# Kernel optimization log

Hardware: AMD Instinct MI355X
Metric: run time of the kernel (lower is better)

The kernel has to match this reference:

```python
import jax, jax.numpy as jnp
import numpy as np

B, L, D, DFF, H, P, TOPK = 64, 321, 512, 2048, 8, 16, 10
LEAKY_ALPHA = 0.5

def setup_inputs() -> dict:
    ks = iter(jax.random.split(jax.random.key(0), 40))
    def w(shape):
        return jax.random.normal(next(ks), shape, dtype=jnp.float32) * 0.02
    inp = {"x": jax.random.normal(next(ks), (B, L, D), dtype=jnp.float32)}
    for name, si, so in [("attn_q", D, D), ("attn_k", D, D), ("attn_v", D, D), ("attn_o", D, D),
                         ("enc", D, D),
                         ("ff1_q", D, DFF), ("ff1_k", D, D), ("ff1_v", D, D), ("ff1_o", DFF, DFF),
                         ("ff2_q", DFF, D), ("ff2_k", DFF, DFF), ("ff2_v", DFF, DFF), ("ff2_o", D, D)]:
        inp[name + "_w"] = w((si, so))
        inp[name + "_b"] = jnp.zeros((so,), dtype=jnp.float32)
    inp["ln_g"] = jnp.ones((DFF,), dtype=jnp.float32)
    inp["ln_b"] = jnp.zeros((DFF,), dtype=jnp.float32)
    inp["n_vars"] = L
    return inp

def _gattn(x, wq, bq, wk, bk, wv, bv, wo, bo):
    Bx, Lx, Dx = x.shape
    E = Dx // H
    q = jax.nn.relu(x @ wq + bq).reshape(Bx, Lx, H, E)
    k = (x @ wk + bk).reshape(Bx, Lx, H, E)
    v = jax.nn.relu(x @ wv + bv).reshape(Bx, Lx, H, E)
    scores = jnp.einsum('blhe,bshe->bhls', q, k)  # [B,H,L,S]
    kth = jax.lax.top_k(scores, TOPK)[0][..., -1:]  # k-th largest per row
    scores = jnp.where(scores < kth, -jnp.inf, scores)
    A = jax.nn.softmax(scores * jnp.float32(1.0 / np.sqrt(E)), axis=-1)
    out = jnp.einsum('bhls,bshd->blhd', A, v).reshape(Bx, Lx, Dx)
    return out @ wo + bo, A

def _pwattn(x, wq, bq, wk, bk, wv, bv, wo, bo):
    N, S = x.shape
    pred = wq.shape[1]
    query = jax.nn.relu(x @ wq + bq)  # [N, pred]
    q = query.reshape(N, pred // P, P)
    k = (x @ wk + bk).reshape(N, S // P, P)
    v = jax.nn.relu(x @ wv + bv).reshape(N, S // P, P)
    A = jax.nn.softmax(jnp.einsum('ble,bse->bls', q, k) * jnp.float32(1.0 / np.sqrt(P)), axis=-1)
    V = jnp.einsum('bls,bse->ble', A, v).reshape(N, pred)
    return query + (V @ wo + bo)

def _layernorm(x, g, b):
    m = x.mean(-1, keepdims=True)
    v = x.var(-1, keepdims=True)
    return (x - m) * jax.lax.rsqrt(v + 1e-5) * g + b

def _forward(x, attn_q_w, attn_q_b, attn_k_w, attn_k_b, attn_v_w, attn_v_b, attn_o_w, attn_o_b,
             enc_w, enc_b,
             ff1_q_w, ff1_q_b, ff1_k_w, ff1_k_b, ff1_v_w, ff1_v_b, ff1_o_w, ff1_o_b,
             ff2_q_w, ff2_q_b, ff2_k_w, ff2_k_b, ff2_v_w, ff2_v_b, ff2_o_w, ff2_o_b,
             ln_g, ln_b, n_vars):
    new_x, A = _gattn(x, attn_q_w, attn_q_b, attn_k_w, attn_k_b, attn_v_w, attn_v_b, attn_o_w, attn_o_b)
    y = x + new_x  # Encoder residual
    y = jax.nn.leaky_relu(y, negative_slope=LEAKY_ALPHA) @ enc_w + enc_b
    y = y.reshape(-1, y.shape[-1])  # [B*L, D]
    y = _layernorm(jax.nn.elu(_pwattn(y, ff1_q_w, ff1_q_b, ff1_k_w, ff1_k_b, ff1_v_w, ff1_v_b, ff1_o_w, ff1_o_b)), ln_g, ln_b)
    y = _pwattn(y, ff2_q_w, ff2_q_b, ff2_k_w, ff2_k_b, ff2_v_w, ff2_v_b, ff2_o_w, ff2_o_b)
    y = y.reshape(-1, n_vars, y.shape[-1])
    return y, A

def reference(x, attn_q_w, attn_q_b, attn_k_w, attn_k_b, attn_v_w, attn_v_b, attn_o_w, attn_o_b,
              enc_w, enc_b,
              ff1_q_w, ff1_q_b, ff1_k_w, ff1_k_b, ff1_v_w, ff1_v_b, ff1_o_w, ff1_o_b,
              ff2_q_w, ff2_q_b, ff2_k_w, ff2_k_b, ff2_v_w, ff2_v_b, ff2_o_w, ff2_o_b,
              ln_g, ln_b, n_vars):
    return _forward(x, attn_q_w, attn_q_b, attn_k_w, attn_k_b, attn_v_w, attn_v_b, attn_o_w, attn_o_b,
                    enc_w, enc_b,
                    ff1_q_w, ff1_q_b, ff1_k_w, ff1_k_b, ff1_v_w, ff1_v_b, ff1_o_w, ff1_o_b,
                    ff2_q_w, ff2_q_b, ff2_k_w, ff2_k_b, ff2_v_w, ff2_v_b, ff2_o_w, ff2_o_b,
                    ln_g, ln_b, n_vars)
```

## Files before the change

kernel.cpp:

```cpp
#include <hip/hip_runtime.h>
#include <hip/hip_bf16.h>
#include <math.h>

#define N_ROWS 20544
#define MP     20608
#define LSEQ   321
#define BB     64
#define HH     8
#define EE     64
#define DD     512
#define DFF    2048

typedef __attribute__((ext_vector_type(8))) short bf16x8;
typedef __attribute__((ext_vector_type(4))) float f32x4;

__device__ inline float bf2f(unsigned short v){ unsigned u = ((unsigned)v) << 16; return __builtin_bit_cast(float, u); }
__device__ inline unsigned short f2bf(float f){ __hip_bfloat16 h = __float2bfloat16(f); return __builtin_bit_cast(unsigned short, h); }
__device__ inline float lo16(unsigned u){ return __builtin_bit_cast(float, u << 16); }
__device__ inline float hi16(unsigned u){ return __builtin_bit_cast(float, u & 0xffff0000u); }
__device__ inline unsigned packbf(float a, float b){ return (unsigned)f2bf(a) | ((unsigned)f2bf(b) << 16); }
__device__ inline void bf8_to_f(uint4 u, float* o){
    o[0]=lo16(u.x); o[1]=hi16(u.x); o[2]=lo16(u.y); o[3]=hi16(u.y);
    o[4]=lo16(u.z); o[5]=hi16(u.z); o[6]=lo16(u.w); o[7]=hi16(u.w);
}

#define GLDS16(gp, lp) __builtin_amdgcn_global_load_lds( \
    (const __attribute__((address_space(1))) unsigned int*)(gp), \
    (__attribute__((address_space(3))) unsigned int*)(lp), 16, 0, 0)

template<int POST>
__global__ __launch_bounds__(256)
void sgemm128_kernel(const float* __restrict__ A, const float* __restrict__ W,
                     const float* __restrict__ bias, float* __restrict__ C,
                     int M, int K, int N)
{
    __shared__ float As[16][132];
    __shared__ float Bs[16][64];
    const int t  = threadIdx.x;
    const int tx = t & 15, ty = t >> 4;
    const int row0 = blockIdx.x << 7, col0 = blockIdx.y << 6;
    const int ar = t >> 2;
    const int ak = (t & 3) << 2;
    const float* Wp = W + (size_t)ty * N + col0 + (tx << 2);
    float acc[8][4] = {};
    for (int k0 = 0; k0 < K; k0 += 16) {
        float4 a0 = make_float4(0.f,0.f,0.f,0.f);
        float4 a1 = make_float4(0.f,0.f,0.f,0.f);
        if (row0 + ar < M)      a0 = *(const float4*)(A + (size_t)(row0 + ar) * K + k0 + ak);
        if (row0 + ar + 64 < M) a1 = *(const float4*)(A + (size_t)(row0 + ar + 64) * K + k0 + ak);
        const float4 wv = *(const float4*)(Wp + (size_t)k0 * N);
        As[ak + 0][ar] = a0.x; As[ak + 1][ar] = a0.y;
        As[ak + 2][ar] = a0.z; As[ak + 3][ar] = a0.w;
        As[ak + 0][ar + 64] = a1.x; As[ak + 1][ar + 64] = a1.y;
        As[ak + 2][ar + 64] = a1.z; As[ak + 3][ar + 64] = a1.w;
        *(float4*)&Bs[ty][tx << 2] = wv;
        __syncthreads();
        #pragma unroll
        for (int kk = 0; kk < 16; ++kk) {
            const float4 aA = *(const float4*)&As[kk][ty << 3];
            const float4 aB = *(const float4*)&As[kk][(ty << 3) + 4];
            const float4 b4 = *(const float4*)&Bs[kk][tx << 2];
            const float a[8] = {aA.x, aA.y, aA.z, aA.w, aB.x, aB.y, aB.z, aB.w};
            const float b[4] = {b4.x, b4.y, b4.z, b4.w};
            #pragma unroll
            for (int i = 0; i < 8; ++i)
                #pragma unroll
                for (int j = 0; j < 4; ++j)
                    acc[i][j] = fmaf(a[i], b[j], acc[i][j]);
        }
        __syncthreads();
    }
    const float4 bi = *(const float4*)(bias + col0 + (tx << 2));
    #pragma unroll
    for (int i = 0; i < 8; ++i) {
        const int row = row0 + (ty << 3) + i;
        if (row < M) {
            float4 c;
            c.x = acc[i][0] + bi.x;
            c.y = acc[i][1] + bi.y;
            c.z = acc[i][2] + bi.z;
            c.w = acc[i][3] + bi.w;
            if (POST == 1) {
                c.x = fmaxf(c.x, 0.f); c.y = fmaxf(c.y, 0.f);
                c.z = fmaxf(c.z, 0.f); c.w = fmaxf(c.w, 0.f);
            }
            *(float4*)(C + (size_t)row * N + col0 + (tx << 2)) = c;
        }
    }
}

__global__ __launch_bounds__(256)
void scores64_kernel(const float* __restrict__ Q, const float* __restrict__ Kx,
                     float* __restrict__ Sc)
{
    const int bh = blockIdx.z, b = bh >> 3, h = bh & 7;
    const int l0 = blockIdx.x << 6, s0 = blockIdx.y << 6;
    __shared__ float qs[64][68];
    __shared__ float ks[64][68];
    const int t = threadIdx.x;
    {
        const int r = t >> 4;
        const int c = (t & 15) << 2;
        #pragma unroll
        for (int i = 0; i < 4; ++i) {
            const int rr = r + (i << 4);
            const int l = l0 + rr, s = s0 + rr;
            float4 qv = make_float4(0.f, 0.f, 0.f, 0.f);
            float4 kv = make_float4(0.f, 0.f, 0.f, 0.f);
            if (l < LSEQ) qv = *(const float4*)(Q + ((size_t)(b * LSEQ + l)) * DD + h * EE + c);
            if (s < LSEQ) kv = *(const float4*)(Kx + ((size_t)(b * LSEQ + s)) * DD + h * EE + c);
            *(float4*)&qs[rr][c] = qv;
            *(float4*)&ks[rr][c] = kv;
        }
    }
    __syncthreads();
    const int tx = t & 15, ty = t >> 4;
    float acc[4][4] = {};
    for (int e = 0; e < EE; e += 4) {
        float4 q4[4], k4[4];
        #pragma unroll
        for (int i = 0; i < 4; ++i) q4[i] = *(const float4*)&qs[ty + (i << 4)][e];
        #pragma unroll
        for (int j = 0; j < 4; ++j) k4[j] = *(const float4*)&ks[tx + (j << 4)][e];
        #pragma unroll
        for (int i = 0; i < 4; ++i)
            #pragma unroll
            for (int j = 0; j < 4; ++j)
                acc[i][j] += q4[i].x * k4[j].x + q4[i].y * k4[j].y + q4[i].z * k4[j].z + q4[i].w * k4[j].w;
    }
    #pragma unroll
    for (int i = 0; i < 4; ++i) {
        const int l = l0 + ty + (i << 4);
        if (l < LSEQ) {
            #pragma unroll
            for (int j = 0; j < 4; ++j) {
                const int s = s0 + tx + (j << 4);
                if (s < LSEQ)
                    Sc[((size_t)bh * LSEQ + l) * LSEQ + s] = acc[i][j];
            }
        }
    }
}

__global__ __launch_bounds__(256)
void topk_softmax_kernel(float* __restrict__ S)
{
    const int wave = threadIdx.x >> 6;
    const int lane = threadIdx.x & 63;
    const size_t row = (size_t)blockIdx.x * 4 + wave;
    float* p = S + row * LSEQ;
    float v[6], w[6];
    #pragma unroll
    for (int j = 0; j < 6; ++j) {
        const int idx = lane + (j << 6);
        v[j] = (idx < LSEQ) ? p[idx] : -INFINITY;
        w[j] = v[j];
    }
    float gmax = 0.f, kth = 0.f;
    #pragma unroll
    for (int it = 0; it < 10; ++it) {
        float m = w[0];
        #pragma unroll
        for (int j = 1; j < 6; ++j) m = fmaxf(m, w[j]);
        #pragma unroll
        for (int off = 32; off > 0; off >>= 1)
            m = fmaxf(m, __shfl_xor(m, off, 64));
        if (it == 0) gmax = m;
        kth = m;
        if (it < 9) {
            int which = -1;
            #pragma unroll
            for (int j = 0; j < 6; ++j)
                if (which < 0 && w[j] == m) which = j;
            const unsigned long long msk = __ballot(which >= 0);
            const int first = __ffsll(msk) - 1;
            if (lane == first) {
                #pragma unroll
                for (int j = 0; j < 6; ++j)
                    if (j == which) w[j] = -INFINITY;
            }
        }
    }
    float ssum = 0.f;
    float e[6];
    #pragma unroll
    for (int j = 0; j < 6; ++j) {
        e[j] = (v[j] >= kth) ? __expf(0.125f * (v[j] - gmax)) : 0.f;
        ssum += e[j];
    }
    #pragma unroll
    for (int off = 32; off > 0; off >>= 1) ssum += __shfl_xor(ssum, off, 64);
    const float inv = 1.f / ssum;
    #pragma unroll
    for (int j = 0; j < 6; ++j) {
        const int idx = lane + (j << 6);
        if (idx < LSEQ) p[idx] = e[j] * inv;
    }
}

__global__ __launch_bounds__(256)
void av_bf16_kernel(const float* __restrict__ A, const unsigned short* __restrict__ V,
                    unsigned short* __restrict__ Out)
{
    const int bh = blockIdx.y, b = bh >> 3, h = bh & 7;
    const int l0 = blockIdx.x << 5;
    __shared__ float As[32][36];
    __shared__ float Vs[32][68];
    const int t = threadIdx.x;
    const int tx = t & 15, ty = t >> 4;
    float acc[2][4] = {};
    for (int s0 = 0; s0 < LSEQ; s0 += 32) {
        {
            const int r = t >> 3, c = (t & 7) << 2;
            const int l = l0 + r;
            const float* ap = A + ((size_t)bh * LSEQ + (l < LSEQ ? l : 0)) * LSEQ + s0 + c;
            #pragma unroll
            for (int jj = 0; jj < 4; ++jj) {
                const int s = s0 + c + jj;
                As[r][c + jj] = (l < LSEQ && s < LSEQ) ? ap[jj] : 0.f;
            }
        }
        #pragma unroll
        for (int pass = 0; pass < 2; ++pass) {
            const int r = (t >> 4) + (pass << 4), c = (t & 15) << 2;
            const int s = s0 + r;
            float4 vv = make_float4(0.f, 0.f, 0.f, 0.f);
            if (s < LSEQ) {
                const ushort4 u = *(const ushort4*)(V + ((size_t)(b * LSEQ + s)) * DD + h * EE + c);
                vv.x = bf2f(u.x); vv.y = bf2f(u.y); vv.z = bf2f(u.z); vv.w = bf2f(u.w);
            }
            *(float4*)&Vs[r][c] = vv;
        }
        __syncthreads();
        #pragma unroll
        for (int ss = 0; ss < 32; ++ss) {
            const float a0 = As[(ty << 1) + 0][ss];
            const float a1 = As[(ty << 1) + 1][ss];
            const float4 vv = *(const float4*)&Vs[ss][tx << 2];
            acc[0][0] = fmaf(a0, vv.x, acc[0][0]);
            acc[0][1] = fmaf(a0, vv.y, acc[0][1]);
            acc[0][2] = fmaf(a0, vv.z, acc[0][2]);
            acc[0][3] = fmaf(a0, vv.w, acc[0][3]);
            acc[1][0] = fmaf(a1, vv.x, acc[1][0]);
            acc[1][1] = fmaf(a1, vv.y, acc[1][1]);
            acc[1][2] = fmaf(a1, vv.z, acc[1][2]);
            acc[1][3] = fmaf(a1, vv.w, acc[1][3]);
        }
        __syncthreads();
    }
    #pragma unroll
    for (int i = 0; i < 2; ++i) {
        const int l = l0 + (ty << 1) + i;
        if (l < LSEQ) {
            ushort4 o;
            o.x = f2bf(acc[i][0]); o.y = f2bf(acc[i][1]);
            o.z = f2bf(acc[i][2]); o.w = f2bf(acc[i][3]);
            *(ushort4*)(Out + ((size_t)(b * LSEQ + l)) * DD + h * EE + (tx << 2)) = o;
        }
    }
}

__global__ __launch_bounds__(256)
void f32_to_bf16_kernel(const float* __restrict__ X, unsigned short* __restrict__ Y,
                        long long nvalid, long long ntotal)
{
    const long long i = ((long long)blockIdx.x * 256 + threadIdx.x) * 4;
    if (i >= ntotal) return;
    float4 v = make_float4(0.f, 0.f, 0.f, 0.f);
    if (i < nvalid) v = *(const float4*)(X + i);
    ushort4 o;
    o.x = f2bf(v.x); o.y = f2bf(v.y); o.z = f2bf(v.z); o.w = f2bf(v.w);
    *(ushort4*)(Y + i) = o;
}

__global__ __launch_bounds__(256)
void transpose_w_kernel(const float* __restrict__ W, unsigned short* __restrict__ Wt,
                        int K, int N)
{
    __shared__ unsigned short s[32][33];
    const int n0 = blockIdx.x << 5, k0 = blockIdx.y << 5;
    const int tx = threadIdx.x & 31, ty = threadIdx.x >> 5;
    #pragma unroll
    for (int i = 0; i < 32; i += 8)
        s[ty + i][tx] = f2bf(W[(size_t)(k0 + ty + i) * N + n0 + tx]);
    __syncthreads();
    #pragma unroll
    for (int i = 0; i < 32; i += 8)
        Wt[(size_t)(n0 + ty + i) * K + k0 + tx] = s[tx][ty + i];
}

template<int RES, int POST, int OUTBF>
__global__ __launch_bounds__(256)
void mgemm_kernel(const unsigned short* __restrict__ A, const unsigned short* __restrict__ Bt,
                  const float* __restrict__ bias, const void* __restrict__ Rres,
                  void* __restrict__ Cout, int M, int K, int N)
{
    __shared__ unsigned short As[128 * 32];
    __shared__ unsigned short Bs[128 * 32];
    const int t = threadIdx.x;
    const int lane = t & 63;
    const int wave = t >> 6;
    const int row0 = blockIdx.y << 7, col0 = blockIdx.x << 7;
    const int wm = (wave >> 1) << 6, wn = (wave & 1) << 6;
    const int r0 = t >> 2;
    const int kh = ((t & 3) ^ ((t >> 3) & 3)) << 3;
    const unsigned short* Ag0 = A + (size_t)(row0 + r0) * K + kh;
    const unsigned short* Ag1 = Ag0 + (size_t)64 * K;
    const unsigned short* Bg0 = Bt + (size_t)(col0 + r0) * K + kh;
    const unsigned short* Bg1 = Bg0 + (size_t)64 * K;
    unsigned short* As0 = As + t * 8;  unsigned short* As1 = As0 + 2048;
    unsigned short* Bs0 = Bs + t * 8;  unsigned short* Bs1 = Bs0 + 2048;
    const int fm = lane & 15, q = lane >> 4;
    int aoff[4], boff[4];
    #pragma unroll
    for (int i = 0; i < 4; ++i) {
        const int Ra = wm + (i << 4) + fm;
        aoff[i] = Ra * 32 + ((q ^ ((Ra >> 1) & 3)) << 3);
        const int Rb = wn + (i << 4) + fm;
        boff[i] = Rb * 32 + ((q ^ ((Rb >> 1) & 3)) << 3);
    }
    f32x4 acc[4][4] = {};
    for (int k0 = 0; k0 < K; k0 += 32) {
        GLDS16(Ag0 + k0, As0);
        GLDS16(Ag1 + k0, As1);
        GLDS16(Bg0 + k0, Bs0);
        GLDS16(Bg1 + k0, Bs1);
        __syncthreads();
        bf16x8 af[4], bfr[4];
        #pragma unroll
        for (int i = 0; i < 4; ++i) {
            af[i]  = *(const bf16x8*)(As + aoff[i]);
            bfr[i] = *(const bf16x8*)(Bs + boff[i]);
        }
        #pragma unroll
        for (int i = 0; i < 4; ++i)
            #pragma unroll
            for (int j = 0; j < 4; ++j)
                acc[i][j] = __builtin_amdgcn_mfma_f32_16x16x32_bf16(af[i], bfr[j], acc[i][j], 0, 0, 0);
        __syncthreads();
    }
    const int qr = (lane >> 4) << 2;
    #pragma unroll
    for (int j = 0; j < 4; ++j) {
        const int gcol = col0 + wn + (j << 4) + fm;
        const float bj = bias[gcol];
        #pragma unroll
        for (int i = 0; i < 4; ++i) {
            const int rb = row0 + wm + (i << 4) + qr;
            #pragma unroll
            for (int rg = 0; rg < 4; ++rg) {
                const int grow = rb + rg;
                if (grow < M) {
                    float c = acc[i][j][rg] + bj;
                    if (RES == 1) c += ((const float*)Rres)[(size_t)grow * N + gcol];
                    if (RES == 2) c += bf2f(((const unsigned short*)Rres)[(size_t)grow * N + gcol]);
                    if (POST == 1) c = fmaxf(c, 0.f);
                    if (POST == 2) c = c >= 0.f ? c : 0.5f * c;
                    if (OUTBF) ((unsigned short*)Cout)[(size_t)grow * N + gcol] = f2bf(c);
                    else       ((float*)Cout)[(size_t)grow * N + gcol] = c;
                }
            }
        }
    }
}

template<int NQ, int NS>
__global__ __launch_bounds__(256)
void pw_attn_bf16(const unsigned short* __restrict__ Q, const unsigned short* __restrict__ Kx,
                  const unsigned short* __restrict__ V, unsigned short* __restrict__ Out)
{
    const long long gid = (long long)blockIdx.x * 256 + threadIdx.x;
    const long long n = gid / NQ;
    const int l = (int)(gid % NQ);
    float qf[16];
    {
        const uint4* qp = (const uint4*)(Q + (size_t)n * NQ * 16 + (size_t)l * 16);
        bf8_to_f(qp[0], qf); bf8_to_f(qp[1], qf + 8);
    }
    const unsigned short* kp = Kx + (size_t)n * NS * 16;
    const unsigned short* vp = V  + (size_t)n * NS * 16;
    float m = -INFINITY, denom = 0.f;
    float acc[16] = {};
    for (int s = 0; s < NS; ++s) {
        float kf[16], vf[16];
        const uint4* kr = (const uint4*)(kp + s * 16);
        bf8_to_f(kr[0], kf); bf8_to_f(kr[1], kf + 8);
        float sc = 0.f;
        #pragma unroll
        for (int j = 0; j < 16; ++j) sc = fmaf(qf[j], kf[j], sc);
        sc *= 0.25f;
        const float nm = fmaxf(m, sc);
        const float fold = __expf(m - nm);
        const float es = __expf(sc - nm);
        denom = denom * fold + es;
        const uint4* vr = (const uint4*)(vp + s * 16);
        bf8_to_f(vr[0], vf); bf8_to_f(vr[1], vf + 8);
        #pragma unroll
        for (int j = 0; j < 16; ++j) acc[j] = acc[j] * fold + es * vf[j];
        m = nm;
    }
    const float inv = 1.f / denom;
    uint4 o0, o1;
    o0.x = packbf(acc[0] * inv,  acc[1] * inv);
    o0.y = packbf(acc[2] * inv,  acc[3] * inv);
    o0.z = packbf(acc[4] * inv,  acc[5] * inv);
    o0.w = packbf(acc[6] * inv,  acc[7] * inv);
    o1.x = packbf(acc[8] * inv,  acc[9] * inv);
    o1.y = packbf(acc[10] * inv, acc[11] * inv);
    o1.z = packbf(acc[12] * inv, acc[13] * inv);
    o1.w = packbf(acc[14] * inv, acc[15] * inv);
    uint4* op = (uint4*)(Out + (size_t)n * NQ * 16 + (size_t)l * 16);
    op[0] = o0; op[1] = o1;
}

__global__ __launch_bounds__(256)
void elu_ln_bf16_kernel(const unsigned short* __restrict__ U, const float* __restrict__ g,
                        const float* __restrict__ bb, unsigned short* __restrict__ Out)
{
    const int row = blockIdx.x;
    const int t = threadIdx.x;
    const size_t base = (size_t)row * DFF + (size_t)t * 8;
    float vals[8];
    {
        const uint4 u4 = *(const uint4*)(U + base);
        bf8_to_f(u4, vals);
    }
    float s = 0.f, sq = 0.f;
    #pragma unroll
    for (int j = 0; j < 8; ++j) {
        const float e = vals[j] > 0.f ? vals[j] : expm1f(vals[j]);
        vals[j] = e;
        s += e; sq += e * e;
    }
    #pragma unroll
    for (int off = 32; off > 0; off >>= 1) {
        s  += __shfl_xor(s,  off, 64);
        sq += __shfl_xor(sq, off, 64);
    }
    __shared__ float rs[4], rq[4];
    const int wave = t >> 6, lane = t & 63;
    if (lane == 0) { rs[wave] = s; rq[wave] = sq; }
    __syncthreads();
    const float ts = rs[0] + rs[1] + rs[2] + rs[3];
    const float tq = rq[0] + rq[1] + rq[2] + rq[3];
    const float mean = ts * (1.f / 2048.f);
    const float var  = tq * (1.f / 2048.f) - mean * mean;
    const float rinv = rsqrtf(var + 1e-5f);
    const float4 g0 = *(const float4*)(g + t * 8);
    const float4 g1 = *(const float4*)(g + t * 8 + 4);
    const float4 b0 = *(const float4*)(bb + t * 8);
    const float4 b1 = *(const float4*)(bb + t * 8 + 4);
    float o[8];
    o[0] = (vals[0] - mean) * rinv * g0.x + b0.x;
    o[1] = (vals[1] - mean) * rinv * g0.y + b0.y;
    o[2] = (vals[2] - mean) * rinv * g0.z + b0.z;
    o[3] = (vals[3] - mean) * rinv * g0.w + b0.w;
    o[4] = (vals[4] - mean) * rinv * g1.x + b1.x;
    o[5] = (vals[5] - mean) * rinv * g1.y + b1.y;
    o[6] = (vals[6] - mean) * rinv * g1.z + b1.z;
    o[7] = (vals[7] - mean) * rinv * g1.w + b1.w;
    uint4 ov;
    ov.x = packbf(o[0], o[1]); ov.y = packbf(o[2], o[3]);
    ov.z = packbf(o[4], o[5]); ov.w = packbf(o[6], o[7]);
    *(uint4*)(Out + base) = ov;
}

extern "C" void kernel_launch(void* const* d_in, const int* in_sizes, int n_in,
                              void* d_out, int out_size, void* d_ws, size_t ws_size,
                              hipStream_t stream)
{
    const float* x        = (const float*)d_in[0];
    const float* attn_q_w = (const float*)d_in[1];
    const float* attn_q_b = (const float*)d_in[2];
    const float* attn_k_w = (const float*)d_in[3];
    const float* attn_k_b = (const float*)d_in[4];
    const float* attn_v_w = (const float*)d_in[5];
    const float* attn_v_b = (const float*)d_in[6];
    const float* attn_o_w = (const float*)d_in[7];
    const float* attn_o_b = (const float*)d_in[8];
    const float* enc_w    = (const float*)d_in[9];
    const float* enc_b    = (const float*)d_in[10];
    const float* ff1_q_w  = (const float*)d_in[11];
    const float* ff1_q_b  = (const float*)d_in[12];
    const float* ff1_k_w  = (const float*)d_in[13];
    const float* ff1_k_b  = (const float*)d_in[14];
    const float* ff1_v_w  = (const float*)d_in[15];
    const float* ff1_v_b  = (const float*)d_in[16];
    const float* ff1_o_w  = (const float*)d_in[17];
    const float* ff1_o_b  = (const float*)d_in[18];
    const float* ff2_q_w  = (const float*)d_in[19];
    const float* ff2_q_b  = (const float*)d_in[20];
    const float* ff2_k_w  = (const float*)d_in[21];
    const float* ff2_k_b  = (const float*)d_in[22];
    const float* ff2_v_w  = (const float*)d_in[23];
    const float* ff2_v_b  = (const float*)d_in[24];
    const float* ff2_o_w  = (const float*)d_in[25];
    const float* ff2_o_b  = (const float*)d_in[26];
    const float* ln_g     = (const float*)d_in[27];
    const float* ln_b     = (const float*)d_in[28];
    (void)in_sizes; (void)n_in; (void)out_size; (void)ws_size;

    float* yout = (float*)d_out;
    float* Aout = yout + (size_t)N_ROWS * DD;

    char* cur = (char*)d_ws;
    auto alloc = [&](size_t bytes) -> void* {
        void* p = (void*)cur;
        cur += (bytes + 255) & ~(size_t)255;
        return p;
    };
    const size_t F32S = (size_t)N_ROWS * DD * 4;
    const size_t BFS  = (size_t)MP * DD * 2;
    const size_t BFG  = (size_t)MP * DFF * 2;
    float* A1 = (float*)alloc(F32S);
    float* A2 = (float*)alloc(F32S);
    unsigned short* xbf = (unsigned short*)alloc(BFS);
    unsigned short* S1 = (unsigned short*)alloc(BFS);
    unsigned short* S2 = (unsigned short*)alloc(BFS);
    unsigned short* S3 = (unsigned short*)alloc(BFS);
    unsigned short* G1 = (unsigned short*)alloc(BFG);
    unsigned short* G2 = (unsigned short*)alloc(BFG);
    unsigned short* G3 = (unsigned short*)alloc(BFG);
    unsigned short* wt_av  = (unsigned short*)alloc((size_t)DD * DD * 2);
    unsigned short* wt_ao  = (unsigned short*)alloc((size_t)DD * DD * 2);
    unsigned short* wt_enc = (unsigned short*)alloc((size_t)DD * DD * 2);
    unsigned short* wt_f1q = (unsigned short*)alloc((size_t)DFF * DD * 2);
    unsigned short* wt_f1k = (unsigned short*)alloc((size_t)DD * DD * 2);
    unsigned short* wt_f1v = (unsigned short*)alloc((size_t)DD * DD * 2);
    unsigned short* wt_f1o = (unsigned short*)alloc((size_t)DFF * DFF * 2);
    unsigned short* wt_f2q = (unsigned short*)alloc((size_t)DD * DFF * 2);
    unsigned short* wt_f2k = (unsigned short*)alloc((size_t)DFF * DFF * 2);
    unsigned short* wt_f2v = (unsigned short*)alloc((size_t)DFF * DFF * 2);
    unsigned short* wt_f2o = (unsigned short*)alloc((size_t)DD * DD * 2);

    const dim3 blk(256);
    const dim3 gq(161, DD / 64);
    const dim3 gm512(DD / 128, MP / 128);
    const dim3 gm2048(DFF / 128, MP / 128);

    transpose_w_kernel<<<dim3(DD/32,  DD/32),  blk, 0, stream>>>(attn_v_w, wt_av,  DD,  DD);
    transpose_w_kernel<<<dim3(DD/32,  DD/32),  blk, 0, stream>>>(attn_o_w, wt_ao,  DD,  DD);
    transpose_w_kernel<<<dim3(DD/32,  DD/32),  blk, 0, stream>>>(enc_w,    wt_enc, DD,  DD);
    transpose_w_kernel<<<dim3(DFF/32, DD/32),  blk, 0, stream>>>(ff1_q_w,  wt_f1q, DD,  DFF);
    transpose_w_kernel<<<dim3(DD/32,  DD/32),  blk, 0, stream>>>(ff1_k_w,  wt_f1k, DD,  DD);
    transpose_w_kernel<<<dim3(DD/32,  DD/32),  blk, 0, stream>>>(ff1_v_w,  wt_f1v, DD,  DD);
    transpose_w_kernel<<<dim3(DFF/32, DFF/32), blk, 0, stream>>>(ff1_o_w,  wt_f1o, DFF, DFF);
    transpose_w_kernel<<<dim3(DD/32,  DFF/32), blk, 0, stream>>>(ff2_q_w,  wt_f2q, DFF, DD);
    transpose_w_kernel<<<dim3(DFF/32, DFF/32), blk, 0, stream>>>(ff2_k_w,  wt_f2k, DFF, DFF);
    transpose_w_kernel<<<dim3(DFF/32, DFF/32), blk, 0, stream>>>(ff2_v_w,  wt_f2v, DFF, DFF);
    transpose_w_kernel<<<dim3(DD/32,  DD/32),  blk, 0, stream>>>(ff2_o_w,  wt_f2o, DD,  DD);
    f32_to_bf16_kernel<<<dim3((MP * DD / 4 + 255) / 256), blk, 0, stream>>>(
        x, xbf, (long long)N_ROWS * DD, (long long)MP * DD);

    sgemm128_kernel<1><<<gq, blk, 0, stream>>>(x, attn_q_w, attn_q_b, A1, N_ROWS, DD, DD);
    sgemm128_kernel<0><<<gq, blk, 0, stream>>>(x, attn_k_w, attn_k_b, A2, N_ROWS, DD, DD);
    mgemm_kernel<0,1,1><<<gm512, blk, 0, stream>>>(xbf, wt_av, attn_v_b, nullptr, S3, N_ROWS, DD, DD);
    scores64_kernel<<<dim3(6, 6, BB * HH), blk, 0, stream>>>(A1, A2, Aout);
    topk_softmax_kernel<<<dim3((BB * HH * LSEQ) / 4), blk, 0, stream>>>(Aout);
    av_bf16_kernel<<<dim3(11, BB * HH), blk, 0, stream>>>(Aout, S3, S1);

    mgemm_kernel<1,2,1><<<gm512, blk, 0, stream>>>(S1, wt_ao, attn_o_b, x, S2, N_ROWS, DD, DD);
    mgemm_kernel<0,0,1><<<gm512, blk, 0, stream>>>(S2, wt_enc, enc_b, nullptr, S1, N_ROWS, DD, DD);
    mgemm_kernel<0,1,1><<<gm2048, blk, 0, stream>>>(S1, wt_f1q, ff1_q_b, nullptr, G1, N_ROWS, DD, DFF);
    mgemm_kernel<0,0,1><<<gm512, blk, 0, stream>>>(S1, wt_f1k, ff1_k_b, nullptr, S2, N_ROWS, DD, DD);
    mgemm_kernel<0,1,1><<<gm512, blk, 0, stream>>>(S1, wt_f1v, ff1_v_b, nullptr, S3, N_ROWS, DD, DD);
    pw_attn_bf16<128,32><<<dim3((N_ROWS * 128) / 256), blk, 0, stream>>>(G1, S2, S3, G2);
    mgemm_kernel<2,0,1><<<gm2048, blk, 0, stream>>>(G2, wt_f1o, ff1_o_b, G1, G3, N_ROWS, DFF, DFF);
    elu_ln_bf16_kernel<<<dim3(N_ROWS), blk, 0, stream>>>(G3, ln_g, ln_b, G1);
    mgemm_kernel<0,1,1><<<gm512, blk, 0, stream>>>(G1, wt_f2q, ff2_q_b, nullptr, S1, N_ROWS, DFF, DD);
    mgemm_kernel<0,0,1><<<gm2048, blk, 0, stream>>>(G1, wt_f2k, ff2_k_b, nullptr, G2, N_ROWS, DFF, DFF);
    mgemm_kernel<0,1,1><<<gm2048, blk, 0, stream>>>(G1, wt_f2v, ff2_v_b, nullptr, G3, N_ROWS, DFF, DFF);
    pw_attn_bf16<32,128><<<dim3((N_ROWS * 32) / 256), blk, 0, stream>>>(S1, G2, G3, S2);
    mgemm_kernel<2,0,0><<<gm512, blk, 0, stream>>>(S2, wt_f2o, ff2_o_b, S1, yout, N_ROWS, DD, DD);
}
```

Before: 2.811 ms.

## Fuse FF Q/K/V projections into one GEMM and add XCD-aware block remapping

Concatenates the transposed Q, K and V weights of each pointwise-attention block into one matrix and runs a single multi-output GEMM kernel. Each column tile routes its results to the right output buffer with its own bias and ReLU. This cuts launches and lets the shared activation tiles be reused across a wider grid. It also remaps linear block IDs so that consecutive tiles land on the same XCD, to improve L2 locality. The risk is extra epilogue branching and a remap that may not match how the hardware actually dispatches blocks to XCDs.

```diff
diff --git a/kernel.cpp b/kernel.cpp
--- a/kernel.cpp
+++ b/kernel.cpp
@@ -27,6 +27,15 @@
 #define GLDS16(gp, lp) __builtin_amdgcn_global_load_lds( \
     (const __attribute__((address_space(1))) unsigned int*)(gp), \
     (__attribute__((address_space(3))) unsigned int*)(lp), 16, 0, 0)
+
+__device__ inline void xcd_remap(int lin, int total, int ncols, int& row0, int& col0)
+{
+    const int per = total >> 3, rem = total & 7;
+    const int xcd = lin & 7, i = lin >> 3;
+    const int g = xcd * per + (xcd < rem ? xcd : rem) + i;
+    row0 = (g / ncols) << 7;
+    col0 = (g % ncols) << 7;
+}
 
 template<int POST>
 __global__ __launch_bounds__(256)
@@ -300,7 +309,8 @@
     const int t = threadIdx.x;
     const int lane = t & 63;
     const int wave = t >> 6;
-    const int row0 = blockIdx.y << 7, col0 = blockIdx.x << 7;
+    int row0, col0;
+    xcd_remap(blockIdx.y * gridDim.x + blockIdx.x, gridDim.x * gridDim.y, gridDim.x, row0, col0);
     const int wm = (wave >> 1) << 6, wn = (wave & 1) << 6;
     const int r0 = t >> 2;
     const int kh = ((t & 3) ^ ((t >> 3) & 3)) << 3;
@@ -358,6 +368,85 @@
                     if (POST == 2) c = c >= 0.f ? c : 0.5f * c;
                     if (OUTBF) ((unsigned short*)Cout)[(size_t)grow * N + gcol] = f2bf(c);
                     else       ((float*)Cout)[(size_t)grow * N + gcol] = c;
+                }
+            }
+        }
+    }
+}
+
+template<int N0, int N1, int N2, int P0, int P1, int P2>
+__global__ __launch_bounds__(256)
+void mgemm3_kernel(const unsigned short* __restrict__ A, const unsigned short* __restrict__ Bt,
+                   const float* __restrict__ b0, const float* __restrict__ b1,
+                   const float* __restrict__ b2,
+                   unsigned short* __restrict__ o0, unsigned short* __restrict__ o1,
+                   unsigned short* __restrict__ o2, int M, int K)
+{
+    __shared__ unsigned short As[128 * 32];
+    __shared__ unsigned short Bs[128 * 32];
+    const int t = threadIdx.x;
+    const int lane = t & 63;
+    const int wave = t >> 6;
+    int row0, col0;
+    xcd_remap(blockIdx.y * gridDim.x + blockIdx.x, gridDim.x * gridDim.y, gridDim.x, row0, col0);
+    const int wm = (wave >> 1) << 6, wn = (wave & 1) << 6;
+    const int r0 = t >> 2;
+    const int kh = ((t & 3) ^ ((t >> 3) & 3)) << 3;
+    const unsigned short* Ag0 = A + (size_t)(row0 + r0) * K + kh;
+    const unsigned short* Ag1 = Ag0 + (size_t)64 * K;
+    const unsigned short* Bg0 = Bt + (size_t)(col0 + r0) * K + kh;
+    const unsigned short* Bg1 = Bg0 + (size_t)64 * K;
+    unsigned short* As0 = As + t * 8;  unsigned short* As1 = As0 + 2048;
+    unsigned short* Bs0 = Bs + t * 8;  unsigned short* Bs1 = Bs0 + 2048;
+    const int fm = lane & 15, q = lane >> 4;
+    int aoff[4], boff[4];
+    #pragma unroll
+    for (int i = 0; i < 4; ++i) {
+        const int Ra = wm + (i << 4) + fm;
+        aoff[i] = Ra * 32 + ((q ^ ((Ra >> 1) & 3)) << 3);
+        const int Rb = wn + (i << 4) + fm;
+        boff[i] = Rb * 32 + ((q ^ ((Rb >> 1) & 3)) << 3);
+    }
+    f32x4 acc[4][4] = {};
+    for (int k0 = 0; k0 < K; k0 += 32) {
+        GLDS16(Ag0 + k0, As0);
+        GLDS16(Ag1 + k0, As1);
+        GLDS16(Bg0 + k0, Bs0);
+        GLDS16(Bg1 + k0, Bs1);
+        __syncthreads();
+        bf16x8 af[4], bfr[4];
+        #pragma unroll
+        for (int i = 0; i < 4; ++i) {
+            af[i]  = *(const bf16x8*)(As + aoff[i]);
+            bfr[i] = *(const bf16x8*)(Bs + boff[i]);
+        }
+        #pragma unroll
+        for (int i = 0; i < 4; ++i)
+            #pragma unroll
+            for (int j = 0; j < 4; ++j)
+                acc[i][j] = __builtin_amdgcn_mfma_f32_16x16x32_bf16(af[i], bfr[j], acc[i][j], 0, 0, 0);
+        __syncthreads();
+    }
+    unsigned short* outp; const float* bp; int segN, segbase, post;
+    if (col0 < N0)           { outp = o0; bp = b0; segN = N0; segbase = 0;       post = P0; }
+    else if (col0 < N0 + N1) { outp = o1; bp = b1; segN = N1; segbase = N0;      post = P1; }
+    else                     { outp = o2; bp = b2; segN = N2; segbase = N0 + N1; post = P2; }
+    const int qr = (lane >> 4) << 2;
+    #pragma unroll
+    for (int j = 0; j < 4; ++j) {
+        const int gcol = col0 + wn + (j << 4) + fm;
+        const int scol = gcol - segbase;
+        const float bj = bp[scol];
+        #pragma unroll
+        for (int i = 0; i < 4; ++i) {
+            const int rb = row0 + wm + (i << 4) + qr;
+            #pragma unroll
+            for (int rg = 0; rg < 4; ++rg) {
+                const int grow = rb + rg;
+                if (grow < M) {
+                    float c = acc[i][j][rg] + bj;
+                    if (post == 1) c = fmaxf(c, 0.f);
+                    outp[(size_t)grow * segN + scol] = f2bf(c);
                 }
             }
         }
@@ -521,34 +610,32 @@
     unsigned short* G1 = (unsigned short*)alloc(BFG);
     unsigned short* G2 = (unsigned short*)alloc(BFG);
     unsigned short* G3 = (unsigned short*)alloc(BFG);
-    unsigned short* wt_av  = (unsigned short*)alloc((size_t)DD * DD * 2);
-    unsigned short* wt_ao  = (unsigned short*)alloc((size_t)DD * DD * 2);
-    unsigned short* wt_enc = (unsigned short*)alloc((size_t)DD * DD * 2);
-    unsigned short* wt_f1q = (unsigned short*)alloc((size_t)DFF * DD * 2);
-    unsigned short* wt_f1k = (unsigned short*)alloc((size_t)DD * DD * 2);
-    unsigned short* wt_f1v = (unsigned short*)alloc((size_t)DD * DD * 2);
-    unsigned short* wt_f1o = (unsigned short*)alloc((size_t)DFF * DFF * 2);
-    unsigned short* wt_f2q = (unsigned short*)alloc((size_t)DD * DFF * 2);
-    unsigned short* wt_f2k = (unsigned short*)alloc((size_t)DFF * DFF * 2);
-    unsigned short* wt_f2v = (unsigned short*)alloc((size_t)DFF * DFF * 2);
-    unsigned short* wt_f2o = (unsigned short*)alloc((size_t)DD * DD * 2);
+    unsigned short* wt_av   = (unsigned short*)alloc((size_t)DD * DD * 2);
+    unsigned short* wt_ao   = (unsigned short*)alloc((size_t)DD * DD * 2);
+    unsigned short* wt_enc  = (unsigned short*)alloc((size_t)DD * DD * 2);
+    unsigned short* wt_f1o  = (unsigned short*)alloc((size_t)DFF * DFF * 2);
+    unsigned short* wt_f2o  = (unsigned short*)alloc((size_t)DD * DD * 2);
+    unsigned short* wt_f1qkv= (unsigned short*)alloc((size_t)(DFF + DD + DD) * DD * 2);
+    unsigned short* wt_f2qkv= (unsigned short*)alloc((size_t)(DD + DFF + DFF) * DFF * 2);
 
     const dim3 blk(256);
     const dim3 gq(161, DD / 64);
     const dim3 gm512(DD / 128, MP / 128);
     const dim3 gm2048(DFF / 128, MP / 128);
+    const dim3 gf1(24, MP / 128);
+    const dim3 gf2(36, MP / 128);
 
     transpose_w_kernel<<<dim3(DD/32,  DD/32),  blk, 0, stream>>>(attn_v_w, wt_av,  DD,  DD);
     transpose_w_kernel<<<dim3(DD/32,  DD/32),  blk, 0, stream>>>(attn_o_w, wt_ao,  DD,  DD);
     transpose_w_kernel<<<dim3(DD/32,  DD/32),  blk, 0, stream>>>(enc_w,    wt_enc, DD,  DD);
-    transpose_w_kernel<<<dim3(DFF/32, DD/32),  blk, 0, stream>>>(ff1_q_w,  wt_f1q, DD,  DFF);
-    transpose_w_kernel<<<dim3(DD/32,  DD/32),  blk, 0, stream>>>(ff1_k_w,  wt_f1k, DD,  DD);
-    transpose_w_kernel<<<dim3(DD/32,  DD/32),  blk, 0, stream>>>(ff1_v_w,  wt_f1v, DD,  DD);
     transpose_w_kernel<<<dim3(DFF/32, DFF/32), blk, 0, stream>>>(ff1_o_w,  wt_f1o, DFF, DFF);
-    transpose_w_kernel<<<dim3(DD/32,  DFF/32), blk, 0, stream>>>(ff2_q_w,  wt_f2q, DFF, DD);
-    transpose_w_kernel<<<dim3(DFF/32, DFF/32), blk, 0, stream>>>(ff2_k_w,  wt_f2k, DFF, DFF);
-    transpose_w_kernel<<<dim3(DFF/32, DFF/32), blk, 0, stream>>>(ff2_v_w,  wt_f2v, DFF, DFF);
     transpose_w_kernel<<<dim3(DD/32,  DD/32),  blk, 0, stream>>>(ff2_o_w,  wt_f2o, DD,  DD);
+    transpose_w_kernel<<<dim3(DFF/32, DD/32),  blk, 0, stream>>>(ff1_q_w, wt_f1qkv,                       DD, DFF);
+    transpose_w_kernel<<<dim3(DD/32,  DD/32),  blk, 0, stream>>>(ff1_k_w, wt_f1qkv + (size_t)DFF * DD,    DD, DD);
+    transpose_w_kernel<<<dim3(DD/32,  DD/32),  blk, 0, stream>>>(ff1_v_w, wt_f1qkv + (size_t)(DFF+DD)*DD, DD, DD);
+    transpose_w_kernel<<<dim3(DD/32,  DFF/32), blk, 0, stream>>>(ff2_q_w, wt_f2qkv,                        DFF, DD);
+    transpose_w_kernel<<<dim3(DFF/32, DFF/32), blk, 0, stream>>>(ff2_k_w, wt_f2qkv + (size_t)DD * DFF,     DFF, DFF);
+    transpose_w_kernel<<<dim3(DFF/32, DFF/32), blk, 0, stream>>>(ff2_v_w, wt_f2qkv + (size_t)(DD+DFF)*DFF, DFF, DFF);
     f32_to_bf16_kernel<<<dim3((MP * DD / 4 + 255) / 256), blk, 0, stream>>>(
         x, xbf, (long long)N_ROWS * DD, (long long)MP * DD);
 
@@ -561,15 +648,13 @@
 
     mgemm_kernel<1,2,1><<<gm512, blk, 0, stream>>>(S1, wt_ao, attn_o_b, x, S2, N_ROWS, DD, DD);
     mgemm_kernel<0,0,1><<<gm512, blk, 0, stream>>>(S2, wt_enc, enc_b, nullptr, S1, N_ROWS, DD, DD);
-    mgemm_kernel<0,1,1><<<gm2048, blk, 0, stream>>>(S1, wt_f1q, ff1_q_b, nullptr, G1, N_ROWS, DD, DFF);
-    mgemm_kernel<0,0,1><<<gm512, blk, 0, stream>>>(S1, wt_f1k, ff1_k_b, nullptr, S2, N_ROWS, DD, DD);
-    mgemm_kernel<0,1,1><<<gm512, blk, 0, stream>>>(S1, wt_f1v, ff1_v_b, nullptr, S3, N_ROWS, DD, DD);
+    mgemm3_kernel<DFF,DD,DD, 1,0,1><<<gf1, blk, 0, stream>>>(S1, wt_f1qkv,
+        ff1_q_b, ff1_k_b, ff1_v_b, G1, S2, S3, N_ROWS, DD);
     pw_attn_bf16<128,32><<<dim3((N_ROWS * 128) / 256), blk, 0, stream>>>(G1, S2, S3, G2);
     mgemm_kernel<2,0,1><<<gm2048, blk, 0, stream>>>(G2, wt_f1o, ff1_o_b, G1, G3, N_ROWS, DFF, DFF);
     elu_ln_bf16_kernel<<<dim3(N_ROWS), blk, 0, stream>>>(G3, ln_g, ln_b, G1);
-    mgemm_kernel<0,1,1><<<gm512, blk, 0, stream>>>(G1, wt_f2q, ff2_q_b, nullptr, S1, N_ROWS, DFF, DD);
-    mgemm_kernel<0,0,1><<<gm2048, blk, 0, stream>>>(G1, wt_f2k, ff2_k_b, nullptr, G2, N_ROWS, DFF, DFF);
-    mgemm_kernel<0,1,1><<<gm2048, blk, 0, stream>>>(G1, wt_f2v, ff2_v_b, nullptr, G3, N_ROWS, DFF, DFF);
+    mgemm3_kernel<DD,DFF,DFF, 1,0,1><<<gf2, blk, 0, stream>>>(G1, wt_f2qkv,
+        ff2_q_b, ff2_k_b, ff2_v_b, S1, G2, G3, N_ROWS, DFF);
     pw_attn_bf16<32,128><<<dim3((N_ROWS * 32) / 256), blk, 0, stream>>>(S1, G2, G3, S2);
     mgemm_kernel<2,0,0><<<gm512, blk, 0, stream>>>(S2, wt_f2o, ff2_o_b, S1, yout, N_ROWS, DD, DD);
 }
```

Result: no change. 2.780 ms (-1.1%).
